# Optimization experiments

Measured on AMD Instinct MI355X. Metric: run time of the kernel, lower is better.

## Reference

```python
import jax, jax.numpy as jnp
import numpy as np

VOC, D, CPR, RELS = 2048, 128, 128, 7
B, DEPTH = 512, 4  # complete binary trees: 2**DEPTH leaves per tree


def setup_inputs() -> dict:
    key = jax.random.key(0)
    ks = jax.random.split(key, 13)
    s = lambda k, shape, fan: jax.random.normal(k, shape, jnp.float32) / np.sqrt(fan)
    return {
        "leaf_ids": jax.random.randint(ks[0], (B, 2, 2 ** DEPTH), 0, VOC),
        "Wv": s(ks[1], (D, VOC), VOC), "bv": jnp.zeros((D,), jnp.float32),
        "Wcps": s(ks[2], (D, 2 * D), 2 * D), "bcps": jnp.zeros((D,), jnp.float32),
        "Wcpst": s(ks[3], (D, D * D), D * D), "bcpst": jnp.zeros((D,), jnp.float32),
        "Wcpr": s(ks[4], (CPR, 2 * D), 2 * D), "bcpr": jnp.zeros((CPR,), jnp.float32),
        "Wcprt": s(ks[5], (CPR, D * D), D * D), "bcprt": jnp.zeros((CPR,), jnp.float32),
        "Wsm": s(ks[6], (RELS, CPR), CPR), "bsm": jnp.zeros((RELS,), jnp.float32),
    }


def reference(leaf_ids, Wv, bv, Wcps, bcps, Wcpst, bcpst, Wcpr, bcpr, Wcprt, bcprt, Wsm, bsm):
    d = Wv.shape[0]
    # leaf embedding: voc(one_hot(idx)) == Wv[:, idx] + bv  -> [B, 2, L, d]
    h = jnp.take(Wv.T, leaf_ids, axis=0) + bv
    # batched level-by-level tree composition (complete binary trees)
    while h.shape[2] > 1:
        l, r = h[:, :, 0::2, :], h[:, :, 1::2, :]
        lin = jnp.concatenate([l, r], axis=-1) @ Wcps.T + bcps
        kron = (l[..., :, None] * r[..., None, :]).reshape(l.shape[:-1] + (d * d,))
        h = jnp.tanh(lin + kron @ Wcpst.T + bcpst)
    lc, rc = h[:, 0, 0, :], h[:, 1, 0, :]  # [B, d] each
    cpr = jnp.concatenate([lc, rc], axis=-1) @ Wcpr.T + bcpr
    kron = (lc[:, :, None] * rc[:, None, :]).reshape(lc.shape[0], d * d)
    act = jax.nn.leaky_relu(cpr + kron @ Wcprt.T + bcprt, 0.01)
    logits = act @ Wsm.T + bsm
    return jax.nn.log_softmax(logits, axis=-1)  # [B, RELS]
```

## Files before the change

kernel.cpp:

```cpp
#include <hip/hip_runtime.h>
#include <hip/hip_bf16.h>
#include <hip/hip_fp16.h>

#define DD    128
#define VOCAB 2048
#define NRELS 7
#define NWF   (130 * 16384)

typedef _Float16 f16;
typedef __attribute__((ext_vector_type(8))) _Float16 f16x8;
typedef __attribute__((ext_vector_type(4))) float    f32x4;

__device__ __forceinline__ float lde(const void* p, size_t i, int bf) {
    if (bf) return (float)((const __hip_bfloat16*)p)[i];
    return ((const float*)p)[i];
}

__device__ __forceinline__ int detect_bf(const unsigned short* wv) {
    int sane = 0;
    #pragma unroll
    for (int i = 0; i < 64; ++i) {
        unsigned e = (wv[i] >> 7) & 0xFFu;
        sane += (e >= 90u && e <= 160u) ? 1 : 0;
    }
    return sane == 64;
}

__global__ void prep_all(const void* Wv, const void* bv,
                         const void* Wcps, const void* bcps,
                         const void* Wcpst, const void* bcpst,
                         const void* Wcpr, const void* bcpr,
                         const void* Wcprt, const void* bcprt,
                         const void* Wsm, const void* bsm,
                         f16* __restrict__ WvT, f16* __restrict__ Wext, f16* __restrict__ Wfin,
                         float* __restrict__ bias_lvl, float* __restrict__ bias_fin,
                         float* __restrict__ Wsm_f, float* __restrict__ bsm_f)
{
    const int bf = detect_bf((const unsigned short*)Wv);
    const int b = blockIdx.x;
    const int tid = threadIdx.x;

    if (b < 64) {
        __shared__ float tile[64][65];
        int vt = b >> 1, dt = b & 1;
        int tx = tid & 63, ty = tid >> 6;
        for (int yy = ty; yy < 64; yy += 4)
            tile[yy][tx] = lde(Wv, (size_t)(dt * 64 + yy) * VOCAB + vt * 64 + tx, bf);
        __syncthreads();
        for (int yy = ty; yy < 64; yy += 4) {
            int v = vt * 64 + yy, d = dt * 64 + tx;
            __builtin_nontemporal_store((f16)(tile[tx][yy] + lde(bv, d, bf)),
                                        &WvT[(size_t)v * DD + d]);
        }
        return;
    }
    if (b >= 2144) {
        if (tid < 128)      bias_lvl[tid] = lde(bcps, tid, bf) + lde(bcpst, tid, bf);
        else if (tid < 256) bias_fin[tid - 128] = lde(bcpr, tid - 128, bf) + lde(bcprt, tid - 128, bf);
        for (int o = tid; o < NRELS * DD; o += 256) Wsm_f[o] = lde(Wsm, o, bf);
        if (tid < NRELS) bsm_f[tid] = lde(bsm, tid, bf);
        return;
    }
    const int bb    = b - 64;
    const int which = bb / 1040;
    const int rem   = bb - which * 1040;
    const int i     = rem >> 3;
    const int n8    = rem & 7;
    const void* Wt = which ? (const void*)Wcprt : (const void*)Wcpst;
    const void* Ws = which ? (const void*)Wcpr  : (const void*)Wcps;
    f16* dst = which ? Wfin : Wext;

    __shared__ float tile[16 * 129];
    #pragma unroll
    for (int it = 0; it < 8; ++it) {
        int idx = it * 256 + tid;
        int rr = idx >> 7, c = idx & 127;
        float v = (i < 128) ? lde(Wt, (size_t)(n8 * 16 + rr) * 16384 + (size_t)i * 128 + c, bf)
                            : lde(Ws, (size_t)(n8 * 16 + rr) * 256 + (size_t)(i - 128) * 128 + c, bf);
        tile[rr * 129 + c] = v;
    }
    __syncthreads();
    f16* out = dst + (size_t)(i * 8 + n8) * 2048;
    #pragma unroll
    for (int it = 0; it < 8; ++it) {
        int o = it * 256 + tid;
        int t = o >> 9, ln = (o >> 3) & 63, e = o & 7;
        __builtin_nontemporal_store((f16)tile[(ln & 15) * 129 + t * 32 + ((ln >> 4) << 3) + e],
                                    &out[o]);
    }
}

template<int BI>
__launch_bounds__(256, 2)
__global__ void gemm_kernel(const f16* __restrict__ hin, const int* __restrict__ ids,
                            const f16* __restrict__ Wf,
                            f16* __restrict__ part, int Mrows, int S)
{
    __shared__ f16 Wb[4][8192];

    const int tid  = threadIdx.x;
    const int lane = tid & 63;
    const int wv   = tid >> 6;
    const int b    = blockIdx.x;
    const int nh   = (b >> 2) & 1;
    const int r    = ((b >> 3) << 2) | (b & 3);
    const int mb   = r / S;
    const int s    = r - mb * S;
    const int m0   = mb * 256;
    const int i0   = s * BI;
    const bool tail = (s == 1 || s == 2);
    const int itail = (s == 1) ? 128 : 129;

    const int mrow = lane & 15;
    const int q    = lane >> 4;
    const int wm   = wv * 64;

    f16x8 rf[4][4];
    int rowL[4];
    #pragma unroll
    for (int mt = 0; mt < 4; ++mt) {
        int p = m0 + wm + mt * 16 + mrow;
        int row = ids ? ids[2 * p + 1] : 2 * p + 1;
        rowL[mt] = ids ? ids[2 * p] : 2 * p;
        #pragma unroll
        for (int t = 0; t < 4; ++t)
            rf[mt][t] = *(const f16x8*)&hin[(size_t)row * DD + t * 32 + q * 8];
    }

    f16 lw[4][BI];
    #pragma unroll
    for (int mt = 0; mt < 4; ++mt) {
        const f16* src = &hin[(size_t)rowL[mt] * DD + i0];
        if constexpr (BI == 16) { *(f16x8*)&lw[mt][0] = *(const f16x8*)src;
                                  *(f16x8*)&lw[mt][8] = *(const f16x8*)(src + 8); }
        else if constexpr (BI == 8) { *(f16x8*)&lw[mt][0] = *(const f16x8*)src; }
        else if constexpr (BI == 4) { *(unsigned long long*)&lw[mt][0] = *(const unsigned long long*)src; }
        else if constexpr (BI == 2) { *(unsigned int*)&lw[mt][0] = *(const unsigned int*)src; }
        else { lw[mt][0] = src[0]; }
    }

    auto stage = [&](int i, int slot) {
        const f16* g = Wf + (size_t)i * 16384 + nh * 8192;
        #pragma unroll
        for (int k = 0; k < 4; ++k) {
            int j = k * 4 + wv;
            const f16* gg = g + (size_t)(j * 64 + lane) * 8;
            f16* l = &Wb[slot][(size_t)(j * 64) * 8];
            __builtin_amdgcn_global_load_lds(
                (const __attribute__((address_space(1))) unsigned int*)gg,
                (__attribute__((address_space(3))) unsigned int*)l, 16, 0, 0);
        }
    };

    stage(i0, 0);
    if (BI > 1)       stage(i0 + 1, 1);
    else if (tail)    stage(itail, 1);
    __syncthreads();

    f32x4 acc[4][4] = {};

#define TSTEP(T, SLOT, KRON, LBV)                                                       \
    {                                                                                   \
        f16x8 wc[4];                                                                    \
        _Pragma("unroll")                                                               \
        for (int nt = 0; nt < 4; ++nt)                                                  \
            wc[nt] = *(const f16x8*)&Wb[SLOT][nt * 2048 + (T) * 512 + lane * 8];        \
        _Pragma("unroll")                                                               \
        for (int mt = 0; mt < 4; ++mt) {                                                \
            f16x8 a = (KRON) ? (LBV[mt] * rf[mt][T]) : rf[mt][T];                       \
            _Pragma("unroll")                                                           \
            for (int nt = 0; nt < 4; ++nt)                                              \
                acc[mt][nt] = __builtin_amdgcn_mfma_f32_16x16x32_f16(a, wc[nt], acc[mt][nt], 0, 0, 0); \
        }                                                                               \
    }

    #pragma unroll
    for (int ii = 0; ii < BI; ++ii) {
        if (ii + 2 < BI)                 stage(i0 + ii + 2, (ii + 2) & 3);
        else if (ii + 2 == BI && tail)   stage(itail, BI & 3);
        f16x8 lb[4];
        #pragma unroll
        for (int mt = 0; mt < 4; ++mt) {
            f16 v = lw[mt][ii];
            #pragma unroll
            for (int e = 0; e < 8; ++e) lb[mt][e] = v;
        }
        TSTEP(0, ii & 3, true, lb); TSTEP(1, ii & 3, true, lb);
        TSTEP(2, ii & 3, true, lb); TSTEP(3, ii & 3, true, lb);
        if (ii & 1) __syncthreads();
    }

    if (tail) {
        const int slot = (BI > 1) ? (BI & 3) : 1;
        if (s == 1) {
            #pragma unroll
            for (int mt = 0; mt < 4; ++mt)
                #pragma unroll
                for (int t = 0; t < 4; ++t)
                    rf[mt][t] = *(const f16x8*)&hin[(size_t)rowL[mt] * DD + t * 32 + q * 8];
        }
        f16x8 dummy[4];
        TSTEP(0, slot, false, dummy); TSTEP(1, slot, false, dummy);
        TSTEP(2, slot, false, dummy); TSTEP(3, slot, false, dummy);
    }
#undef TSTEP

    f16* pb = part + ((size_t)s * Mrows + m0) * DD + nh * 64;
    #pragma unroll
    for (int mt = 0; mt < 4; ++mt)
        #pragma unroll
        for (int nt = 0; nt < 4; ++nt) {
            int colg = nt * 16 + mrow;
            #pragma unroll
            for (int rr = 0; rr < 4; ++rr) {
                int rowl = wm + mt * 16 + q * 4 + rr;
                pb[(size_t)rowl * DD + colg] = (f16)acc[mt][nt][rr];
            }
        }
}

__global__ void epi_level(const f16* __restrict__ part, const float* __restrict__ bias,
                          f16* __restrict__ hout, int Mrows, int S)
{
    int idx = (blockIdx.x * 256 + threadIdx.x) * 8;
    size_t stride = (size_t)Mrows * DD;
    float sum[8] = {};
    for (int s2 = 0; s2 < S; ++s2) {
        f16x8 v = *(const f16x8*)&part[(size_t)s2 * stride + idx];
        #pragma unroll
        for (int e = 0; e < 8; ++e) sum[e] += (float)v[e];
    }
    int n = idx & 127;
    f16x8 o;
    #pragma unroll
    for (int e = 0; e < 8; ++e) o[e] = (f16)tanhf(sum[e] + bias[n + e]);
    *(f16x8*)&hout[idx] = o;
}

__global__ void fin_epi(const f16* __restrict__ part, const float* __restrict__ bias,
                        const float* __restrict__ Wsm_f, const float* __restrict__ bsm_f,
                        const unsigned short* __restrict__ wv_raw, void* __restrict__ outp, int S)
{
    int lane = threadIdx.x & 63;
    int wv = threadIdx.x >> 6;
    int p = blockIdx.x * 4 + wv;
    size_t stride = (size_t)512 * DD;
    const f16* base = part + (size_t)p * DD;
    float a0 = 0.f, a1 = 0.f;
    for (int s2 = 0; s2 < S; ++s2) {
        a0 += (float)base[(size_t)s2 * stride + lane];
        a1 += (float)base[(size_t)s2 * stride + 64 + lane];
    }
    a0 += bias[lane];      a1 += bias[64 + lane];
    a0 = (a0 > 0.f) ? a0 : 0.01f * a0;
    a1 = (a1 > 0.f) ? a1 : 0.01f * a1;
    float lg[NRELS];
    #pragma unroll
    for (int r = 0; r < NRELS; ++r) {
        float pr = a0 * Wsm_f[r * DD + lane] + a1 * Wsm_f[r * DD + 64 + lane];
        #pragma unroll
        for (int d = 1; d < 64; d <<= 1) pr += __shfl_xor(pr, d, 64);
        lg[r] = pr + bsm_f[r];
    }
    float mx = lg[0];
    #pragma unroll
    for (int r = 1; r < NRELS; ++r) mx = fmaxf(mx, lg[r]);
    float se = 0.f;
    #pragma unroll
    for (int r = 0; r < NRELS; ++r) se += expf(lg[r] - mx);
    float lse = logf(se) + mx;
    if (lane < NRELS) {
        float v = lg[lane] - lse;
        if (detect_bf(wv_raw)) ((__hip_bfloat16*)outp)[p * NRELS + lane] = __float2bfloat16(v);
        else                   ((float*)outp)[p * NRELS + lane] = v;
    }
}

extern "C" void kernel_launch(void* const* d_in, const int* in_sizes, int n_in,
                              void* d_out, int out_size, void* d_ws, size_t ws_size,
                              hipStream_t stream)
{
    const int* ids = (const int*)d_in[0];

    char* ws = (char*)d_ws;
    f16*   part     = (f16*)ws;
    f16*   h1       = (f16*)(ws + ((size_t)32 << 20));
    f16*   h2       = (f16*)(ws + ((size_t)34 << 20));
    f16*   h3       = (f16*)(ws + ((size_t)35 << 20));
    f16*   h4       = (f16*)(ws + ((size_t)35 << 20) + (512 << 10));
    f16*   WvT      = (f16*)(ws + ((size_t)36 << 20));
    f16*   Wext     = (f16*)(ws + ((size_t)36 << 20) + (512 << 10));
    f16*   Wfin     = Wext + (size_t)NWF;
    float* bias_lvl = (float*)(Wfin + (size_t)NWF);
    float* bias_fin = bias_lvl + 128;
    float* Wsm_f    = bias_fin + 128;
    float* bsm_f    = Wsm_f + NRELS * DD;

    if (ws_size < ((size_t)48 << 20)) return;

    prep_all<<<2145, 256, 0, stream>>>(d_in[1], d_in[2], d_in[3], d_in[4], d_in[5], d_in[6],
                                       d_in[7], d_in[8], d_in[9], d_in[10], d_in[11], d_in[12],
                                       WvT, Wext, Wfin, bias_lvl, bias_fin, Wsm_f, bsm_f);

    gemm_kernel<8><<<1024, 256, 0, stream>>>(WvT, ids, Wext, part, 8192, 16);
    epi_level<<<512, 256, 0, stream>>>(part, bias_lvl, h1, 8192, 16);
    gemm_kernel<8><<<512, 256, 0, stream>>>(h1, nullptr, Wext, part, 4096, 16);
    epi_level<<<256, 256, 0, stream>>>(part, bias_lvl, h2, 4096, 16);
    gemm_kernel<4><<<512, 256, 0, stream>>>(h2, nullptr, Wext, part, 2048, 32);
    epi_level<<<128, 256, 0, stream>>>(part, bias_lvl, h3, 2048, 32);
    gemm_kernel<4><<<256, 256, 0, stream>>>(h3, nullptr, Wext, part, 1024, 32);
    epi_level<<<64, 256, 0, stream>>>(part, bias_lvl, h4, 1024, 32);
    gemm_kernel<2><<<256, 256, 0, stream>>>(h4, nullptr, Wfin, part, 512, 64);
    fin_epi<<<128, 256, 0, stream>>>(part, bias_fin, Wsm_f, bsm_f,
                                     (const unsigned short*)d_in[1], d_out, 64);
}
```

Before: 260.1 us.

## Load weight fragments directly from global memory instead of LDS staging

Drops the 4-slot LDS ring buffer that was filled with async global_load_lds and the periodic block barriers. Each wave now reads its MFMA B-fragments straight from global (L2/cache) per step, and the MFMA sections are wrapped in s_setprio. This removes LDS traffic, LDS allocation and barriers, which may raise occupancy. The cost is that the four waves each read the same weight slice redundantly from cache, and global load latency is no longer hidden by the explicit prefetch.

```diff
diff --git a/kernel.cpp b/kernel.cpp
--- a/kernel.cpp
+++ b/kernel.cpp
@@ -96,8 +96,6 @@
                             const f16* __restrict__ Wf,
                             f16* __restrict__ part, int Mrows, int S)
 {
-    __shared__ f16 Wb[4][8192];
-
     const int tid  = threadIdx.x;
     const int lane = tid & 63;
     const int wv   = tid >> 6;
@@ -139,32 +137,16 @@
         else { lw[mt][0] = src[0]; }
     }
 
-    auto stage = [&](int i, int slot) {
-        const f16* g = Wf + (size_t)i * 16384 + nh * 8192;
-        #pragma unroll
-        for (int k = 0; k < 4; ++k) {
-            int j = k * 4 + wv;
-            const f16* gg = g + (size_t)(j * 64 + lane) * 8;
-            f16* l = &Wb[slot][(size_t)(j * 64) * 8];
-            __builtin_amdgcn_global_load_lds(
-                (const __attribute__((address_space(1))) unsigned int*)gg,
-                (__attribute__((address_space(3))) unsigned int*)l, 16, 0, 0);
-        }
-    };
-
-    stage(i0, 0);
-    if (BI > 1)       stage(i0 + 1, 1);
-    else if (tail)    stage(itail, 1);
-    __syncthreads();
+    const f16* __restrict__ wb = Wf + (size_t)nh * 8192 + (size_t)lane * 8;
 
     f32x4 acc[4][4] = {};
 
-#define TSTEP(T, SLOT, KRON, LBV)                                                       \
+#define TSTEP(T, WBI, KRON, LBV)                                                        \
     {                                                                                   \
         f16x8 wc[4];                                                                    \
         _Pragma("unroll")                                                               \
         for (int nt = 0; nt < 4; ++nt)                                                  \
-            wc[nt] = *(const f16x8*)&Wb[SLOT][nt * 2048 + (T) * 512 + lane * 8];        \
+            wc[nt] = *(const f16x8*)&(WBI)[nt * 2048 + (T) * 512];                      \
         _Pragma("unroll")                                                               \
         for (int mt = 0; mt < 4; ++mt) {                                                \
             f16x8 a = (KRON) ? (LBV[mt] * rf[mt][T]) : rf[mt][T];                       \
@@ -176,8 +158,7 @@
 
     #pragma unroll
     for (int ii = 0; ii < BI; ++ii) {
-        if (ii + 2 < BI)                 stage(i0 + ii + 2, (ii + 2) & 3);
-        else if (ii + 2 == BI && tail)   stage(itail, BI & 3);
+        const f16* __restrict__ wbi = wb + (size_t)(i0 + ii) * 16384;
         f16x8 lb[4];
         #pragma unroll
         for (int mt = 0; mt < 4; ++mt) {
@@ -185,13 +166,14 @@
             #pragma unroll
             for (int e = 0; e < 8; ++e) lb[mt][e] = v;
         }
-        TSTEP(0, ii & 3, true, lb); TSTEP(1, ii & 3, true, lb);
-        TSTEP(2, ii & 3, true, lb); TSTEP(3, ii & 3, true, lb);
-        if (ii & 1) __syncthreads();
+        __builtin_amdgcn_s_setprio(1);
+        TSTEP(0, wbi, true, lb); TSTEP(1, wbi, true, lb);
+        TSTEP(2, wbi, true, lb); TSTEP(3, wbi, true, lb);
+        __builtin_amdgcn_s_setprio(0);
     }
 
     if (tail) {
-        const int slot = (BI > 1) ? (BI & 3) : 1;
+        const f16* __restrict__ wbi = wb + (size_t)itail * 16384;
         if (s == 1) {
             #pragma unroll
             for (int mt = 0; mt < 4; ++mt)
@@ -200,8 +182,10 @@
                     rf[mt][t] = *(const f16x8*)&hin[(size_t)rowL[mt] * DD + t * 32 + q * 8];
         }
         f16x8 dummy[4];
-        TSTEP(0, slot, false, dummy); TSTEP(1, slot, false, dummy);
-        TSTEP(2, slot, false, dummy); TSTEP(3, slot, false, dummy);
+        __builtin_amdgcn_s_setprio(1);
+        TSTEP(0, wbi, false, dummy); TSTEP(1, wbi, false, dummy);
+        TSTEP(2, wbi, false, dummy); TSTEP(3, wbi, false, dummy);
+        __builtin_amdgcn_s_setprio(0);
     }
 #undef TSTEP
 
```

Result: slower. 275.2 us (+5.8%).
